# Optimization experiments

Measured on AMD Instinct MI355X. Metric: run time of the kernel, lower is better.

Reference implementation:

```python
import jax, jax.numpy as jnp
import numpy as np

N_NODES = 100000
N_EDGES = 3200000
IN_DIM = 8
HID = 64
N_LAYERS = 3
LN_EPS = 1e-5


def setup_inputs() -> dict:
    key = jax.random.key(0)
    ks = jax.random.split(key, 10)
    x = jax.random.normal(ks[0], (N_NODES, IN_DIM), dtype=jnp.float32)
    edge_src = jax.random.randint(ks[1], (N_EDGES,), 0, N_NODES, dtype=jnp.int32)
    edge_dst = jax.random.randint(ks[2], (N_EDGES,), 0, N_NODES, dtype=jnp.int32)
    # parameters
    W_in = jax.random.normal(ks[3], (HID, IN_DIM), dtype=jnp.float32) * 0.1
    b_in = jnp.zeros((HID,), dtype=jnp.float32)
    Ws_self = jax.random.normal(ks[4], (N_LAYERS, HID, HID), dtype=jnp.float32) * 0.1
    Ws_neigh = jax.random.normal(ks[5], (N_LAYERS, HID, HID), dtype=jnp.float32) * 0.1
    biases = jnp.zeros((N_LAYERS, HID), dtype=jnp.float32)
    gammas = jnp.ones((N_LAYERS, HID), dtype=jnp.float32)
    betas = jnp.zeros((N_LAYERS, HID), dtype=jnp.float32)
    return {"x": x, "edge_src": edge_src, "edge_dst": edge_dst,
            "W_in": W_in, "b_in": b_in, "Ws_self": Ws_self,
            "Ws_neigh": Ws_neigh, "biases": biases,
            "gammas": gammas, "betas": betas}


def _layer_norm(h, gamma, beta):
    mu = jnp.mean(h, axis=-1, keepdims=True)
    var = jnp.mean((h - mu) ** 2, axis=-1, keepdims=True)
    return (h - mu) * jax.lax.rsqrt(var + LN_EPS) * gamma + beta


def reference(x, edge_src, edge_dst, W_in, b_in, Ws_self, Ws_neigh, biases, gammas, betas):
    n = x.shape[0]
    # deg[v] = number of neighbors gathered for node v (edges ending at v)
    deg = jax.ops.segment_sum(jnp.ones_like(edge_dst, dtype=jnp.float32), edge_dst,
                              num_segments=n)  # (n,)
    inv_deg = jnp.where(deg > 0, 1.0 / jnp.maximum(deg, 1.0), 0.0)[:, None]

    h = jax.nn.relu(x @ W_in.T + b_in)  # (n, HID); dropout is identity in eval
    for l in range(N_LAYERS):
        # mean neighbor features: gather + scatter-add + normalize
        neigh_sum = jax.ops.segment_sum(h[edge_src], edge_dst, num_segments=n)
        neigh_mean = neigh_sum * inv_deg  # zero rows where deg==0, as in original
        h_self = h @ Ws_self[l].T
        h_neigh = neigh_mean @ Ws_neigh[l].T  # linear has no bias -> 0 when deg==0
        h_l = _layer_norm(h_self + h_neigh + biases[l], gammas[l], betas[l])
        h = h + jax.nn.relu(h_l)  # residual from DrBCEncoder
    return h
```

## Files before the change

kernel.cpp:

```cpp
#include <hip/hip_runtime.h>

#define HID 64
#define BSHIFT 9
#define NPB 512
#define P3TILE 4096
#define HISTB 512

typedef unsigned int uint;
typedef unsigned short ushort;
typedef unsigned char uchar;
typedef float f32x4 __attribute__((ext_vector_type(4)));
typedef short bf16x8 __attribute__((ext_vector_type(8)));

__device__ inline ushort f2b(float f) {
    uint u = __float_as_uint(f);
    return (ushort)((u + 0x7fffu + ((u >> 16) & 1u)) >> 16);
}

__device__ inline float b2f(ushort b) { return __uint_as_float((uint)b << 16); }

__device__ inline void accf8(float* a, uint4 hv) {
    auto p0 = __builtin_amdgcn_cvt_pk_f32_fp8(hv.x, false);
    auto p1 = __builtin_amdgcn_cvt_pk_f32_fp8(hv.x, true);
    auto p2 = __builtin_amdgcn_cvt_pk_f32_fp8(hv.y, false);
    auto p3 = __builtin_amdgcn_cvt_pk_f32_fp8(hv.y, true);
    auto p4 = __builtin_amdgcn_cvt_pk_f32_fp8(hv.z, false);
    auto p5 = __builtin_amdgcn_cvt_pk_f32_fp8(hv.z, true);
    auto p6 = __builtin_amdgcn_cvt_pk_f32_fp8(hv.w, false);
    auto p7 = __builtin_amdgcn_cvt_pk_f32_fp8(hv.w, true);
    a[0] += p0[0];  a[1] += p0[1];
    a[2] += p1[0];  a[3] += p1[1];
    a[4] += p2[0];  a[5] += p2[1];
    a[6] += p3[0];  a[7] += p3[1];
    a[8] += p4[0];  a[9] += p4[1];
    a[10] += p5[0]; a[11] += p5[1];
    a[12] += p6[0]; a[13] += p6[1];
    a[14] += p7[0]; a[15] += p7[1];
}

__device__ inline uchar f2fp8(float f) {
    return (uchar)(__builtin_amdgcn_cvt_pk_fp8_f32(f, f, 0, false) & 0xff);
}


__global__ __launch_bounds__(256) void hist_input(const int* __restrict__ dst,
                                                  int* __restrict__ bcnt, int e, int nb,
                                                  const float* __restrict__ x,
                                                  const float* __restrict__ W_in,
                                                  const float* __restrict__ b_in,
                                                  ushort* __restrict__ hb,
                                                  uchar* __restrict__ h8, int n,
                                                  int inb) {
    __shared__ float smem[576];
    int t = threadIdx.x;
    int b = blockIdx.x;
    if (b < HISTB) {
        int* lh = (int*)smem;
        lh[t] = 0;
        __syncthreads();
        for (int i = b * 256 + t; i < e; i += HISTB * 256)
            atomicAdd(&lh[dst[i] >> BSHIFT], 1);
        __syncthreads();
        if (t < nb && lh[t]) atomicAdd(&bcnt[t], lh[t]);
        return;
    }
    int ib = b - HISTB;
    float* WlT = smem;
    float* bl = smem + 512;
    for (int i = t; i < 512; i += 256) {
        int j = i >> 3, k = i & 7;
        WlT[k * 64 + j] = W_in[i];
    }
    if (t < 64) bl[t] = b_in[t];
    __syncthreads();
    int total2 = n * 32;
    for (int i = ib * 256 + t; i < total2; i += inb * 256) {
        int v = i >> 5;
        int jp = i & 31;
        int j0 = jp * 2, j1 = jp * 2 + 1;
        const float* xr = x + (size_t)v * 8;
        float s0 = bl[j0], s1 = bl[j1];
#pragma unroll
        for (int k = 0; k < 8; ++k) {
            float xv = xr[k];
            s0 += xv * WlT[k * 64 + j0];
            s1 += xv * WlT[k * 64 + j1];
        }
        float o0 = fmaxf(s0, 0.0f), o1 = fmaxf(s1, 0.0f);
        ((uint*)hb)[i] = (uint)f2b(o0) | ((uint)f2b(o1) << 16);
        int pk = __builtin_amdgcn_cvt_pk_fp8_f32(o0, o1, 0, false);
        *(ushort*)&h8[(size_t)2 * i] = (ushort)(pk & 0xffff);
    }
}

__global__ void bucket_scan(const int* __restrict__ bcnt, int* __restrict__ bbase,
                            int* __restrict__ bcur, int* __restrict__ offsets,
                            int e, int nb, int n) {
    __shared__ int sd[256];
    int t = threadIdx.x;
    int v = (t < nb) ? bcnt[t] : 0;
    sd[t] = v;
    __syncthreads();
    for (int off = 1; off < 256; off <<= 1) {
        int u = (t >= off) ? sd[t - off] : 0;
        __syncthreads();
        sd[t] += u;
        __syncthreads();
    }
    int excl = t ? sd[t - 1] : 0;
    if (t < nb) { bbase[t] = excl; bcur[t] = excl; }
    if (t == nb) bbase[t] = e;
    if (t == 0) offsets[n] = e;
}

__global__ __launch_bounds__(256) void partition(const int* __restrict__ src,
                                                 const int* __restrict__ dst,
                                                 int* __restrict__ bcur,
                                                 int* __restrict__ pair, int e, int nb) {
    __shared__ int lh[256], cb[256];
    int t = threadIdx.x;
    int base = blockIdx.x * P3TILE;
    lh[t] = 0;
    __syncthreads();
    int s[16], d[16], r[16];
    if (base + P3TILE <= e) {
        const int4* s4 = (const int4*)(src + base);
        const int4* d4 = (const int4*)(dst + base);
#pragma unroll
        for (int k = 0; k < 4; ++k) {
            int4 sv = s4[t * 4 + k];
            int4 dv = d4[t * 4 + k];
            s[k * 4 + 0] = sv.x; s[k * 4 + 1] = sv.y;
            s[k * 4 + 2] = sv.z; s[k * 4 + 3] = sv.w;
            d[k * 4 + 0] = dv.x; d[k * 4 + 1] = dv.y;
            d[k * 4 + 2] = dv.z; d[k * 4 + 3] = dv.w;
        }
#pragma unroll
        for (int k = 0; k < 16; ++k)
            r[k] = atomicAdd(&lh[d[k] >> BSHIFT], 1);
        __syncthreads();
        if (t < nb && lh[t]) cb[t] = atomicAdd(&bcur[t], lh[t]);
        __syncthreads();
#pragma unroll
        for (int k = 0; k < 16; ++k)
            pair[cb[d[k] >> BSHIFT] + r[k]] = (s[k] << BSHIFT) | (d[k] & (NPB - 1));
    } else {
#pragma unroll
        for (int k = 0; k < 16; ++k) {
            int i = base + t * 16 + k;
            if (i < e) {
                s[k] = src[i];
                d[k] = dst[i];
                r[k] = atomicAdd(&lh[d[k] >> BSHIFT], 1);
            }
        }
        __syncthreads();
        if (t < nb && lh[t]) cb[t] = atomicAdd(&bcur[t], lh[t]);
        __syncthreads();
#pragma unroll
        for (int k = 0; k < 16; ++k) {
            int i = base + t * 16 + k;
            if (i < e)
                pair[cb[d[k] >> BSHIFT] + r[k]] = (s[k] << BSHIFT) | (d[k] & (NPB - 1));
        }
    }
}

__global__ __launch_bounds__(1024) void build_csr(const int* __restrict__ pair,
                                                  const int* __restrict__ bbase,
                                                  int* __restrict__ offsets,
                                                  float* __restrict__ invdeg,
                                                  int* __restrict__ col, int n) {
    __shared__ int bins[NPB], cur[NPB], sd[NPB];
    int b = blockIdx.x, t = threadIdx.x;
    int cbase = bbase[b], cend = bbase[b + 1];
    int v0 = b << BSHIFT;
    if (t < NPB) bins[t] = 0;
    __syncthreads();
    for (int i = cbase + t; i < cend; i += 1024)
        atomicAdd(&bins[pair[i] & (NPB - 1)], 1);
    __syncthreads();
    int d = (t < NPB) ? bins[t] : 0;
    if (t < NPB) sd[t] = d;
    __syncthreads();
    for (int off = 1; off < NPB; off <<= 1) {
        int u = (t < NPB && t >= off) ? sd[t - off] : 0;
        __syncthreads();
        if (t < NPB) sd[t] += u;
        __syncthreads();
    }
    if (t < NPB) {
        int excl = sd[t] - d;
        cur[t] = excl;
        int v = v0 + t;
        if (v < n) {
            offsets[v] = cbase + excl;
            invdeg[v] = d > 0 ? 1.0f / (float)d : 0.0f;
        }
    }
    __syncthreads();
    for (int i = cbase + t; i < cend; i += 1024) {
        int p = pair[i];
        int pos = atomicAdd(&cur[p & (NPB - 1)], 1);
        col[cbase + pos] = p >> BSHIFT;
    }
}


__global__ __launch_bounds__(256) void prep_w(const float* __restrict__ Ws,
                                              const float* __restrict__ Wn,
                                              ushort* __restrict__ Wcat, int total) {
    int i = blockIdx.x * 256 + threadIdx.x;
    if (i >= total) return;
    int l = i >> 13;
    int r = i & 8191;
    int j = r >> 7;
    int k = r & 127;
    float v = (k < 64) ? Ws[l * 4096 + j * 64 + k] : Wn[l * 4096 + j * 64 + (k - 64)];
    Wcat[i] = f2b(v);
}


__global__ __launch_bounds__(256) void aggregate_fp8(const uchar* __restrict__ h8,
                                                     ushort* __restrict__ nmb,
                                                     const int* __restrict__ offsets,
                                                     const int* __restrict__ col,
                                                     const float* __restrict__ invdeg,
                                                     int n) {
    int t = threadIdx.x, lane = t & 63, wid = t >> 6;
    int q = lane >> 4;
    int fl = lane & 15;
    int e4 = lane & 3;
    int sl = (lane >> 2) & 3;
    int nwaves = gridDim.x * 4;
    int ngrp = (n + 3) >> 2;
    for (int w = blockIdx.x * 4 + wid; w < ngrp; w += nwaves) {
        int v = w * 4 + q;
        bool valid = v < n;
        int vv = valid ? v : n - 1;
        int o0 = offsets[vv], o1 = offsets[vv + 1];
        int deg = o1 - o0;
        const int* cp = col + o0;
        int deg16 = deg & ~15;
        float acc[16];
#pragma unroll
        for (int k = 0; k < 16; ++k) acc[k] = 0.f;
        for (int base = 0; base < deg16; base += 16) {
            int idx16 = cp[base + fl];
#pragma unroll
            for (int jj = 0; jj < 16; jj += 4) {
                int ne = __shfl(idx16, q * 16 + jj + sl);
                uint4 hv = *(const uint4*)&h8[(size_t)ne * HID + e4 * 16];
                accf8(acc, hv);
            }
        }
        for (int jj = 0; jj < 16; jj += 4) {
            if (deg16 + jj >= deg) break;
            int j = deg16 + jj + sl;
            if (j < deg) {
                int ne = cp[j];
                uint4 hv = *(const uint4*)&h8[(size_t)ne * HID + e4 * 16];
                accf8(acc, hv);
            }
        }
#pragma unroll
        for (int k = 0; k < 16; ++k) {
            acc[k] += __shfl_xor(acc[k], 4);
            acc[k] += __shfl_xor(acc[k], 8);
        }
        if (valid && sl == 0) {
            float s = invdeg[vv];
            uint4 lo, hi;
            lo.x = (uint)f2b(acc[0] * s) | ((uint)f2b(acc[1] * s) << 16);
            lo.y = (uint)f2b(acc[2] * s) | ((uint)f2b(acc[3] * s) << 16);
            lo.z = (uint)f2b(acc[4] * s) | ((uint)f2b(acc[5] * s) << 16);
            lo.w = (uint)f2b(acc[6] * s) | ((uint)f2b(acc[7] * s) << 16);
            hi.x = (uint)f2b(acc[8] * s) | ((uint)f2b(acc[9] * s) << 16);
            hi.y = (uint)f2b(acc[10] * s) | ((uint)f2b(acc[11] * s) << 16);
            hi.z = (uint)f2b(acc[12] * s) | ((uint)f2b(acc[13] * s) << 16);
            hi.w = (uint)f2b(acc[14] * s) | ((uint)f2b(acc[15] * s) << 16);
            *(uint4*)&nmb[(size_t)v * HID + e4 * 16] = lo;
            *(uint4*)&nmb[(size_t)v * HID + e4 * 16 + 8] = hi;
        }
    }
}


__global__ __launch_bounds__(256) void transform_mfma(
    const ushort* __restrict__ hbm, const ushort* __restrict__ nmb,
    ushort* __restrict__ hbout, uchar* __restrict__ h8out,
    float* __restrict__ outF, const ushort* __restrict__ Wcat,
    const float* __restrict__ bias, const float* __restrict__ gamma,
    const float* __restrict__ beta, int n, int last) {
    int t = threadIdx.x, lane = t & 63, wid = t >> 6;
    int c = lane & 15, g = lane >> 4;
    bf16x8 Bf[4][4];
#pragma unroll
    for (int tt = 0; tt < 4; ++tt)
#pragma unroll
        for (int s = 0; s < 4; ++s)
            Bf[s][tt] = *(const bf16x8*)&Wcat[(tt * 16 + c) * 128 + s * 32 + g * 8];
    float bcol[4], gcol[4], btc[4];
#pragma unroll
    for (int tt = 0; tt < 4; ++tt) {
        bcol[tt] = bias[tt * 16 + c];
        gcol[tt] = gamma[tt * 16 + c];
        btc[tt] = beta[tt * 16 + c];
    }
    int ntiles = (n + 15) >> 4;
    int nw = gridDim.x * 4;
    for (int tile = blockIdx.x * 4 + wid; tile < ntiles; tile += nw) {
        int m0 = tile << 4;
        int node = m0 + c;
        int nodeL = node < n ? node : n - 1;
        bf16x8 Af[4];
#pragma unroll
        for (int s = 0; s < 2; ++s)
            Af[s] = *(const bf16x8*)&hbm[(size_t)nodeL * HID + s * 32 + g * 8];
#pragma unroll
        for (int s = 0; s < 2; ++s)
            Af[2 + s] = *(const bf16x8*)&nmb[(size_t)nodeL * HID + s * 32 + g * 8];
        f32x4 acc[4] = {{0, 0, 0, 0}, {0, 0, 0, 0}, {0, 0, 0, 0}, {0, 0, 0, 0}};
#pragma unroll
        for (int tt = 0; tt < 4; ++tt)
#pragma unroll
            for (int s = 0; s < 4; ++s)
                acc[tt] = __builtin_amdgcn_mfma_f32_16x16x32_bf16(Af[s], Bf[s][tt],
                                                                 acc[tt], 0, 0, 0);
        float v[4][4];
#pragma unroll
        for (int tt = 0; tt < 4; ++tt)
#pragma unroll
            for (int r = 0; r < 4; ++r) v[tt][r] = acc[tt][r] + bcol[tt];
#pragma unroll
        for (int r = 0; r < 4; ++r) {
            float s = v[0][r] + v[1][r] + v[2][r] + v[3][r];
            s += __shfl_xor(s, 1);
            s += __shfl_xor(s, 2);
            s += __shfl_xor(s, 4);
            s += __shfl_xor(s, 8);
            float mu = s * (1.0f / 64.0f);
            float ss = 0.f;
#pragma unroll
            for (int tt = 0; tt < 4; ++tt) {
                float d = v[tt][r] - mu;
                ss += d * d;
            }
            ss += __shfl_xor(ss, 1);
            ss += __shfl_xor(ss, 2);
            ss += __shfl_xor(ss, 4);
            ss += __shfl_xor(ss, 8);
            float inv = rsqrtf(ss * (1.0f / 64.0f) + 1e-5f);
            int nr = m0 + g * 4 + r;
            if (nr < n) {
#pragma unroll
                for (int tt = 0; tt < 4; ++tt) {
                    int j = tt * 16 + c;
                    float hl = (v[tt][r] - mu) * inv * gcol[tt] + btc[tt];
                    float hv = b2f(hbm[(size_t)nr * HID + j]);
                    float o = hv + fmaxf(hl, 0.0f);
                    if (last) {
                        outF[(size_t)nr * HID + j] = o;
                    } else {
                        hbout[(size_t)nr * HID + j] = f2b(o);
                        h8out[(size_t)nr * HID + j] = f2fp8(o);
                    }
                }
            }
        }
    }
}


extern "C" void kernel_launch(void* const* d_in, const int* in_sizes, int n_in,
                              void* d_out, int out_size, void* d_ws, size_t ws_size,
                              hipStream_t stream) {
    const float* x = (const float*)d_in[0];
    const int* edge_src = (const int*)d_in[1];
    const int* edge_dst = (const int*)d_in[2];
    const float* W_in = (const float*)d_in[3];
    const float* b_in = (const float*)d_in[4];
    const float* Ws_self = (const float*)d_in[5];
    const float* Ws_neigh = (const float*)d_in[6];
    const float* biases = (const float*)d_in[7];
    const float* gammas = (const float*)d_in[8];
    const float* betas = (const float*)d_in[9];
    float* out = (float*)d_out;

    int n = in_sizes[0] / 8;
    int e = in_sizes[1];
    int nb = (n + NPB - 1) >> BSHIFT;

    char* w = (char*)d_ws;
    size_t off = 0;
    auto carve = [&](size_t bytes) -> void* {
        void* p = w + off;
        off = (off + bytes + 255) & ~(size_t)255;
        return p;
    };
    int* offsets = (int*)carve((size_t)(n + 1) * 4);
    float* invdeg = (float*)carve((size_t)n * 4);
    int* bcnt = (int*)carve(1024 * 4);
    int* bbase = (int*)carve(1024 * 4);
    int* bcur = (int*)carve(1024 * 4);
    int* col = (int*)carve((size_t)e * 4);
    int* pairbuf = (int*)carve((size_t)e * 4);
    ushort* hb = (ushort*)carve((size_t)n * HID * 2);
    ushort* nm16 = (ushort*)carve((size_t)n * HID * 2);
    uchar* h8 = (uchar*)carve((size_t)n * HID);
    ushort* Wcat = (ushort*)carve(3 * 64 * 128 * 2);
    (void)ws_size;

    hipMemsetAsync(bcnt, 0, 1024 * 4, stream);
    hist_input<<<HISTB + 2048, 256, 0, stream>>>(edge_dst, bcnt, e, nb,
                                                 x, W_in, b_in, hb, h8, n, 2048);
    bucket_scan<<<1, 256, 0, stream>>>(bcnt, bbase, bcur, offsets, e, nb, n);
    partition<<<(e + P3TILE - 1) / P3TILE, 256, 0, stream>>>(edge_src, edge_dst, bcur,
                                                            pairbuf, e, nb);
    build_csr<<<nb, 1024, 0, stream>>>(pairbuf, bbase, offsets, invdeg, col, n);
    prep_w<<<(3 * 8192 + 255) / 256, 256, 0, stream>>>(Ws_self, Ws_neigh, Wcat, 3 * 8192);

    int tfblocks = ((n + 15) / 16 + 3) / 4;
    for (int l = 0; l < 3; ++l) {
        aggregate_fp8<<<2048, 256, 0, stream>>>(h8, nm16, offsets, col, invdeg, n);
        transform_mfma<<<tfblocks, 256, 0, stream>>>(hb, nm16, hb, h8, out,
                                                     Wcat + (size_t)l * 8192,
                                                     biases + l * 64, gammas + l * 64,
                                                     betas + l * 64, n, l == 2 ? 1 : 0);
    }
}
```

Measured before the change: 306.9 us.

## Split neighbor aggregation into two source-half passes for L2 locality

The CSR build now sorts each node's neighbor list by whether the source index falls in the lower or upper half of the node range, and records a per-node mid pointer. Aggregation runs as two kernels: the first sums only lower-half sources into an fp16 partial buffer, and the second adds upper-half sources and applies the mean scale. Each pass therefore gathers from only half of the fp8 feature table, which is meant to fit better in cache. The cost is an extra launch per layer, a round trip of the partial buffer through memory (reusing the pair buffer when it is large enough), and fp16 rounding of the partial sums. The column-index load is also prefetched one tile ahead.

```diff
diff --git a/kernel.cpp b/kernel.cpp
--- a/kernel.cpp
+++ b/kernel.cpp
@@ -3,6 +3,7 @@
 #define HID 64
 #define BSHIFT 9
 #define NPB 512
+#define NB2 1024
 #define P3TILE 4096
 #define HISTB 512
 
@@ -18,6 +19,15 @@
 }
 
 __device__ inline float b2f(ushort b) { return __uint_as_float((uint)b << 16); }
+
+__device__ inline ushort f2h(float f) {
+    _Float16 h = (_Float16)f;
+    return __builtin_bit_cast(ushort, h);
+}
+
+__device__ inline float h2f(ushort u) {
+    return (float)__builtin_bit_cast(_Float16, u);
+}
 
 __device__ inline void accf8(float* a, uint4 hv) {
     auto p0 = __builtin_amdgcn_cvt_pk_f32_fp8(hv.x, false);
@@ -169,39 +179,47 @@
 __global__ __launch_bounds__(1024) void build_csr(const int* __restrict__ pair,
                                                   const int* __restrict__ bbase,
                                                   int* __restrict__ offsets,
+                                                  int* __restrict__ mid,
                                                   float* __restrict__ invdeg,
-                                                  int* __restrict__ col, int n) {
-    __shared__ int bins[NPB], cur[NPB], sd[NPB];
+                                                  int* __restrict__ col, int n,
+                                                  int half) {
+    __shared__ int bins[NB2], cur[NB2], sd[NB2];
     int b = blockIdx.x, t = threadIdx.x;
     int cbase = bbase[b], cend = bbase[b + 1];
     int v0 = b << BSHIFT;
-    if (t < NPB) bins[t] = 0;
-    __syncthreads();
-    for (int i = cbase + t; i < cend; i += 1024)
-        atomicAdd(&bins[pair[i] & (NPB - 1)], 1);
-    __syncthreads();
-    int d = (t < NPB) ? bins[t] : 0;
-    if (t < NPB) sd[t] = d;
-    __syncthreads();
-    for (int off = 1; off < NPB; off <<= 1) {
-        int u = (t < NPB && t >= off) ? sd[t - off] : 0;
-        __syncthreads();
-        if (t < NPB) sd[t] += u;
-        __syncthreads();
-    }
-    if (t < NPB) {
-        int excl = sd[t] - d;
-        cur[t] = excl;
-        int v = v0 + t;
+    bins[t] = 0;
+    __syncthreads();
+    for (int i = cbase + t; i < cend; i += 1024) {
+        int p = pair[i];
+        int b2 = ((p & (NPB - 1)) << 1) | ((p >> BSHIFT) >= half);
+        atomicAdd(&bins[b2], 1);
+    }
+    __syncthreads();
+    int d = bins[t];
+    sd[t] = d;
+    __syncthreads();
+    for (int off = 1; off < NB2; off <<= 1) {
+        int u = (t >= off) ? sd[t - off] : 0;
+        __syncthreads();
+        sd[t] += u;
+        __syncthreads();
+    }
+    int excl = sd[t] - d;
+    cur[t] = excl;
+    if ((t & 1) == 0) {
+        int v = v0 + (t >> 1);
         if (v < n) {
             offsets[v] = cbase + excl;
-            invdeg[v] = d > 0 ? 1.0f / (float)d : 0.0f;
+            mid[v] = cbase + sd[t];
+            int dtot = d + bins[t + 1];
+            invdeg[v] = dtot > 0 ? 1.0f / (float)dtot : 0.0f;
         }
     }
     __syncthreads();
     for (int i = cbase + t; i < cend; i += 1024) {
         int p = pair[i];
-        int pos = atomicAdd(&cur[p & (NPB - 1)], 1);
+        int b2 = ((p & (NPB - 1)) << 1) | ((p >> BSHIFT) >= half);
+        int pos = atomicAdd(&cur[b2], 1);
         col[cbase + pos] = p >> BSHIFT;
     }
 }
@@ -221,12 +239,14 @@
 }
 
 
-__global__ __launch_bounds__(256) void aggregate_fp8(const uchar* __restrict__ h8,
-                                                     ushort* __restrict__ nmb,
-                                                     const int* __restrict__ offsets,
-                                                     const int* __restrict__ col,
-                                                     const float* __restrict__ invdeg,
-                                                     int n) {
+template <int PHASE>
+__global__ __launch_bounds__(256) void aggregate_ph(const uchar* __restrict__ h8,
+                                                    const int* __restrict__ offsets,
+                                                    const int* __restrict__ mid,
+                                                    const int* __restrict__ col,
+                                                    const float* __restrict__ invdeg,
+                                                    ushort* __restrict__ nmP,
+                                                    ushort* __restrict__ nmb, int n) {
     int t = threadIdx.x, lane = t & 63, wid = t >> 6;
     int q = lane >> 4;
     int fl = lane & 15;
@@ -238,26 +258,57 @@
         int v = w * 4 + q;
         bool valid = v < n;
         int vv = valid ? v : n - 1;
-        int o0 = offsets[vv], o1 = offsets[vv + 1];
-        int deg = o1 - o0;
-        const int* cp = col + o0;
-        int deg16 = deg & ~15;
+        int s0, e0;
+        if (PHASE == 0) {
+            s0 = offsets[vv];
+            e0 = mid[vv];
+        } else {
+            s0 = mid[vv];
+            e0 = offsets[vv + 1];
+        }
+        int dg = e0 - s0;
+        const int* cp = col + s0;
+        int deg16 = dg & ~15;
         float acc[16];
-#pragma unroll
-        for (int k = 0; k < 16; ++k) acc[k] = 0.f;
+        if (PHASE == 0) {
+#pragma unroll
+            for (int k = 0; k < 16; ++k) acc[k] = 0.f;
+        } else {
+            uint4 plo = *(const uint4*)&nmP[(size_t)vv * HID + e4 * 16];
+            uint4 phi = *(const uint4*)&nmP[(size_t)vv * HID + e4 * 16 + 8];
+            acc[0] = h2f((ushort)(plo.x & 0xffff)) * 0.25f;
+            acc[1] = h2f((ushort)(plo.x >> 16)) * 0.25f;
+            acc[2] = h2f((ushort)(plo.y & 0xffff)) * 0.25f;
+            acc[3] = h2f((ushort)(plo.y >> 16)) * 0.25f;
+            acc[4] = h2f((ushort)(plo.z & 0xffff)) * 0.25f;
+            acc[5] = h2f((ushort)(plo.z >> 16)) * 0.25f;
+            acc[6] = h2f((ushort)(plo.w & 0xffff)) * 0.25f;
+            acc[7] = h2f((ushort)(plo.w >> 16)) * 0.25f;
+            acc[8] = h2f((ushort)(phi.x & 0xffff)) * 0.25f;
+            acc[9] = h2f((ushort)(phi.x >> 16)) * 0.25f;
+            acc[10] = h2f((ushort)(phi.y & 0xffff)) * 0.25f;
+            acc[11] = h2f((ushort)(phi.y >> 16)) * 0.25f;
+            acc[12] = h2f((ushort)(phi.z & 0xffff)) * 0.25f;
+            acc[13] = h2f((ushort)(phi.z >> 16)) * 0.25f;
+            acc[14] = h2f((ushort)(phi.w & 0xffff)) * 0.25f;
+            acc[15] = h2f((ushort)(phi.w >> 16)) * 0.25f;
+        }
+        int idx16 = 0;
+        if (deg16 > 0) idx16 = cp[fl];
         for (int base = 0; base < deg16; base += 16) {
-            int idx16 = cp[base + fl];
+            int ci = idx16;
+            if (base + 16 < deg16) idx16 = cp[base + 16 + fl];
 #pragma unroll
             for (int jj = 0; jj < 16; jj += 4) {
-                int ne = __shfl(idx16, q * 16 + jj + sl);
+                int ne = __shfl(ci, q * 16 + jj + sl);
                 uint4 hv = *(const uint4*)&h8[(size_t)ne * HID + e4 * 16];
                 accf8(acc, hv);
             }
         }
         for (int jj = 0; jj < 16; jj += 4) {
-            if (deg16 + jj >= deg) break;
+            if (deg16 + jj >= dg) break;
             int j = deg16 + jj + sl;
-            if (j < deg) {
+            if (j < dg) {
                 int ne = cp[j];
                 uint4 hv = *(const uint4*)&h8[(size_t)ne * HID + e4 * 16];
                 accf8(acc, hv);
@@ -269,18 +320,31 @@
             acc[k] += __shfl_xor(acc[k], 8);
         }
         if (valid && sl == 0) {
-            float s = invdeg[vv];
             uint4 lo, hi;
-            lo.x = (uint)f2b(acc[0] * s) | ((uint)f2b(acc[1] * s) << 16);
-            lo.y = (uint)f2b(acc[2] * s) | ((uint)f2b(acc[3] * s) << 16);
-            lo.z = (uint)f2b(acc[4] * s) | ((uint)f2b(acc[5] * s) << 16);
-            lo.w = (uint)f2b(acc[6] * s) | ((uint)f2b(acc[7] * s) << 16);
-            hi.x = (uint)f2b(acc[8] * s) | ((uint)f2b(acc[9] * s) << 16);
-            hi.y = (uint)f2b(acc[10] * s) | ((uint)f2b(acc[11] * s) << 16);
-            hi.z = (uint)f2b(acc[12] * s) | ((uint)f2b(acc[13] * s) << 16);
-            hi.w = (uint)f2b(acc[14] * s) | ((uint)f2b(acc[15] * s) << 16);
-            *(uint4*)&nmb[(size_t)v * HID + e4 * 16] = lo;
-            *(uint4*)&nmb[(size_t)v * HID + e4 * 16 + 8] = hi;
+            if (PHASE == 0) {
+                lo.x = (uint)f2h(acc[0]) | ((uint)f2h(acc[1]) << 16);
+                lo.y = (uint)f2h(acc[2]) | ((uint)f2h(acc[3]) << 16);
+                lo.z = (uint)f2h(acc[4]) | ((uint)f2h(acc[5]) << 16);
+                lo.w = (uint)f2h(acc[6]) | ((uint)f2h(acc[7]) << 16);
+                hi.x = (uint)f2h(acc[8]) | ((uint)f2h(acc[9]) << 16);
+                hi.y = (uint)f2h(acc[10]) | ((uint)f2h(acc[11]) << 16);
+                hi.z = (uint)f2h(acc[12]) | ((uint)f2h(acc[13]) << 16);
+                hi.w = (uint)f2h(acc[14]) | ((uint)f2h(acc[15]) << 16);
+                *(uint4*)&nmP[(size_t)v * HID + e4 * 16] = lo;
+                *(uint4*)&nmP[(size_t)v * HID + e4 * 16 + 8] = hi;
+            } else {
+                float s = invdeg[vv];
+                lo.x = (uint)f2b(acc[0] * s) | ((uint)f2b(acc[1] * s) << 16);
+                lo.y = (uint)f2b(acc[2] * s) | ((uint)f2b(acc[3] * s) << 16);
+                lo.z = (uint)f2b(acc[4] * s) | ((uint)f2b(acc[5] * s) << 16);
+                lo.w = (uint)f2b(acc[6] * s) | ((uint)f2b(acc[7] * s) << 16);
+                hi.x = (uint)f2b(acc[8] * s) | ((uint)f2b(acc[9] * s) << 16);
+                hi.y = (uint)f2b(acc[10] * s) | ((uint)f2b(acc[11] * s) << 16);
+                hi.z = (uint)f2b(acc[12] * s) | ((uint)f2b(acc[13] * s) << 16);
+                hi.w = (uint)f2b(acc[14] * s) | ((uint)f2b(acc[15] * s) << 16);
+                *(uint4*)&nmb[(size_t)v * HID + e4 * 16] = lo;
+                *(uint4*)&nmb[(size_t)v * HID + e4 * 16 + 8] = hi;
+            }
         }
     }
 }
@@ -390,6 +454,7 @@
     int n = in_sizes[0] / 8;
     int e = in_sizes[1];
     int nb = (n + NPB - 1) >> BSHIFT;
+    int half = (n + 1) >> 1;
 
     char* w = (char*)d_ws;
     size_t off = 0;
@@ -399,6 +464,7 @@
         return p;
     };
     int* offsets = (int*)carve((size_t)(n + 1) * 4);
+    int* mid = (int*)carve((size_t)(n + 1) * 4);
     float* invdeg = (float*)carve((size_t)n * 4);
     int* bcnt = (int*)carve(1024 * 4);
     int* bbase = (int*)carve(1024 * 4);
@@ -409,6 +475,9 @@
     ushort* nm16 = (ushort*)carve((size_t)n * HID * 2);
     uchar* h8 = (uchar*)carve((size_t)n * HID);
     ushort* Wcat = (ushort*)carve(3 * 64 * 128 * 2);
+    size_t needP = (size_t)n * HID * 2;
+    ushort* nmP = ((size_t)e * 4 >= needP) ? (ushort*)pairbuf
+                                           : (ushort*)carve(needP);
     (void)ws_size;
 
     hipMemsetAsync(bcnt, 0, 1024 * 4, stream);
@@ -417,12 +486,16 @@
     bucket_scan<<<1, 256, 0, stream>>>(bcnt, bbase, bcur, offsets, e, nb, n);
     partition<<<(e + P3TILE - 1) / P3TILE, 256, 0, stream>>>(edge_src, edge_dst, bcur,
                                                             pairbuf, e, nb);
-    build_csr<<<nb, 1024, 0, stream>>>(pairbuf, bbase, offsets, invdeg, col, n);
+    build_csr<<<nb, 1024, 0, stream>>>(pairbuf, bbase, offsets, mid, invdeg, col, n,
+                                       half);
     prep_w<<<(3 * 8192 + 255) / 256, 256, 0, stream>>>(Ws_self, Ws_neigh, Wcat, 3 * 8192);
 
     int tfblocks = ((n + 15) / 16 + 3) / 4;
     for (int l = 0; l < 3; ++l) {
-        aggregate_fp8<<<2048, 256, 0, stream>>>(h8, nm16, offsets, col, invdeg, n);
+        aggregate_ph<0><<<2048, 256, 0, stream>>>(h8, offsets, mid, col, invdeg,
+                                                  nmP, nm16, n);
+        aggregate_ph<1><<<2048, 256, 0, stream>>>(h8, offsets, mid, col, invdeg,
+                                                  nmP, nm16, n);
         transform_mfma<<<tfblocks, 256, 0, stream>>>(hb, nm16, hb, h8, out,
                                                      Wcat + (size_t)l * 8192,
                                                      biases + l * 64, gammas + l * 64,
```

After: 373.3 us. +21.6%, slower.
